# Optimization experiments

Measured on AMD Instinct MI355X. Metric: run time of the kernel, lower is better.

The kernel has to match this reference:

```python
import jax, jax.numpy as jnp
import numpy as np

NUM_HEADS = 12
SIZE_PER_HEAD = 64


def setup_inputs() -> dict:
    key = jax.random.key(0)
    ks = jax.random.split(key, 4)
    B, S, D = 4, 2048, NUM_HEADS * SIZE_PER_HEAD
    std = 0.02
    return {
        "x": jax.random.normal(ks[0], (B, S, D), dtype=jnp.float32),
        "Wq": jax.random.normal(ks[1], (D, D), dtype=jnp.float32) * std,
        "bq": jnp.zeros((D,), dtype=jnp.float32),
        "Wk": jax.random.normal(ks[2], (D, D), dtype=jnp.float32) * std,
        "bk": jnp.zeros((D,), dtype=jnp.float32),
        "Wv": jax.random.normal(ks[3], (D, D), dtype=jnp.float32) * std,
        "bv": jnp.zeros((D,), dtype=jnp.float32),
        "mask": jnp.ones((B, S), dtype=jnp.int32),
    }


def reference(x, Wq, bq, Wk, bk, Wv, bv, mask):
    B, S, Dm = x.shape
    H, Dh = NUM_HEADS, SIZE_PER_HEAD
    # QKV projections (no activation, per defaults)
    q = (x @ Wq + bq).reshape(B, S, H, Dh)
    k = (x @ Wk + bk).reshape(B, S, H, Dh)
    v = (x @ Wv + bv).reshape(B, S, H, Dh)
    # scaled dot-product scores [B, H, F, T]
    scores = jnp.einsum("bfhd,bthd->bhft", q, k) / jnp.sqrt(
        jnp.asarray(Dh, dtype=x.dtype)
    )
    # additive mask: (1 - mask) * -10000, broadcast over heads and F
    adder = (1.0 - mask.astype(x.dtype))[:, None, None, :] * -10000.0
    probs = jax.nn.softmax(scores + adder, axis=-1)
    # dropout is identity at inference (training=None)
    ctx = jnp.einsum("bhft,bthd->bfhd", probs, v)
    return ctx.reshape(B, S, H * Dh)
```

## Files before the change

kernel.cpp:

```cpp
#include <hip/hip_runtime.h>
#include <cstdint>
#include <cstddef>

#define B_  4
#define S_  2048
#define H_  12
#define DH  64
#define DM  768

typedef unsigned short u16;
typedef __bf16 bf16x8 __attribute__((ext_vector_type(8)));
typedef float f32x4 __attribute__((ext_vector_type(4)));

__device__ __forceinline__ u16 f2bf(float f) {
  unsigned u = __float_as_uint(f);
  u += 0x7FFFu + ((u >> 16) & 1u);
  return (u16)(u >> 16);
}

__device__ __forceinline__ void gl16(const u16* g, u16* l) {
  __builtin_amdgcn_global_load_lds((const __attribute__((address_space(1))) void*)g,
                                   (__attribute__((address_space(3))) void*)l,
                                   16, 0, 0);
}

__global__ __launch_bounds__(256) void k_prep(const float* __restrict__ x, u16* __restrict__ xb,
                                              const int* __restrict__ mask, int* __restrict__ mflags,
                                              const float* __restrict__ Wq, const float* __restrict__ Wk,
                                              const float* __restrict__ Wv, u16* __restrict__ Wt) {
  const int bid = blockIdx.x;
  if (bid < 6144) {
    int i = bid * 256 + threadIdx.x;
    const float4 v = ((const float4*)x)[i];
    ushort4 o;
    o.x = f2bf(v.x); o.y = f2bf(v.y); o.z = f2bf(v.z); o.w = f2bf(v.w);
    ((ushort4*)xb)[i] = o;
    if (bid < 64) {
      __shared__ int f;
      if (threadIdx.x == 0) f = 0;
      __syncthreads();
      if (threadIdx.x < 128 && mask[bid * 128 + threadIdx.x] != 1) f = 1;
      __syncthreads();
      if (threadIdx.x == 0) mflags[bid] = f;
    }
  } else {
    const int b2 = bid - 6144;
    const int z = b2 / 576, rem = b2 % 576;
    const int by = rem / 24, bx = rem % 24;
    const float* W = z == 0 ? Wq : (z == 1 ? Wk : Wv);
    u16* o = Wt + (size_t)z * DM * DM;
    __shared__ float t[32][33];
    const int xx = threadIdx.x & 31, yy = threadIdx.x >> 5;
    const int n0 = bx * 32, k0 = by * 32;
#pragma unroll
    for (int i = 0; i < 4; i++)
      t[yy + i*8][xx] = W[(size_t)(k0 + yy + i*8)*DM + n0 + xx];
    __syncthreads();
#pragma unroll
    for (int i = 0; i < 4; i++)
      o[(size_t)(n0 + yy + i*8)*DM + k0 + xx] = f2bf(t[xx][yy + i*8]);
  }
}

__global__ __launch_bounds__(256, 2) void k_qkv(const u16* __restrict__ Xb, const u16* __restrict__ Wt,
                                                const float* __restrict__ bq, const float* __restrict__ bk,
                                                const float* __restrict__ bv, u16* __restrict__ QKV,
                                                u16* __restrict__ Vt) {
  const int n0 = blockIdx.x * 256, m0 = blockIdx.y * 128;
  const int mat = blockIdx.x / 3;
  const int n0r = n0 - mat * 768;
  const float* bias = mat == 0 ? bq : (mat == 1 ? bk : bv);
  __shared__ __align__(16) u16 Al[2*128*32];
  __shared__ __align__(16) u16 Bl[2*256*32];
  const int tid = threadIdx.x, w = tid >> 6, l = tid & 63, l15 = l & 15, quad = l >> 4;
  const int wm = w & 1, wn = w >> 1;
  f32x4 acc[4][8];
#pragma unroll
  for (int i = 0; i < 4; i++)
#pragma unroll
    for (int j = 0; j < 8; j++) acc[i][j] = f32x4{0.f, 0.f, 0.f, 0.f};

  int aoff[2], boff[4];
#pragma unroll
  for (int i = 0; i < 2; i++) {
    int c = tid + i*256;
    int r = c >> 2, s = c & 3, sl = s ^ ((r ^ (r >> 2)) & 3);
    aoff[i] = r*DM + sl*8;
  }
#pragma unroll
  for (int i = 0; i < 4; i++) {
    int c = tid + i*256;
    int r = c >> 2, s = c & 3, sl = s ^ ((r ^ (r >> 2)) & 3);
    boff[i] = r*DM + sl*8;
  }
  const u16* ap = Xb + (size_t)m0 * DM;
  const u16* bp = Wt + (size_t)n0 * DM;

#define STAGE(kt) {                                             \
    int ab = ((kt) & 1) * 4096, bb = ((kt) & 1) * 8192;         \
    _Pragma("unroll")                                           \
    for (int i = 0; i < 2; i++)                                 \
      gl16(ap + (kt)*32 + aoff[i], Al + ab + (tid + i*256)*8);  \
    _Pragma("unroll")                                           \
    for (int i = 0; i < 4; i++)                                 \
      gl16(bp + (kt)*32 + boff[i], Bl + bb + (tid + i*256)*8);  \
  }

  STAGE(0)
  for (int kt = 0; kt < DM/32; ++kt) {
    __syncthreads();
    if (kt + 1 < DM/32) STAGE(kt+1)
    const int ab = (kt & 1) * 4096, bb = (kt & 1) * 8192;
    bf16x8 af[4], bfr[8];
#pragma unroll
    for (int mt = 0; mt < 4; mt++) {
      int row = wm*64 + mt*16 + l15;
      int ph = quad ^ ((row ^ (row >> 2)) & 3);
      af[mt] = *(const bf16x8*)(Al + ab + row*32 + ph*8);
    }
#pragma unroll
    for (int nt = 0; nt < 8; nt++) {
      int row = wn*128 + nt*16 + l15;
      int ph = quad ^ ((row ^ (row >> 2)) & 3);
      bfr[nt] = *(const bf16x8*)(Bl + bb + row*32 + ph*8);
    }
#pragma unroll
    for (int mt = 0; mt < 4; mt++)
#pragma unroll
      for (int nt = 0; nt < 8; nt++)
        acc[mt][nt] = __builtin_amdgcn_mfma_f32_16x16x32_bf16(af[mt], bfr[nt], acc[mt][nt], 0, 0, 0);
  }
#undef STAGE

  float b8[8];
#pragma unroll
  for (int nt = 0; nt < 8; nt++) b8[nt] = bias[n0r + wn*128 + nt*16 + l15];

  if (mat == 2) {
#pragma unroll
    for (int mt = 0; mt < 4; mt++) {
      int gm = m0 + wm*64 + mt*16 + quad*4;
      int b = gm >> 11, t = gm & 2047;
#pragma unroll
      for (int nt = 0; nt < 8; nt++) {
        int ng = n0r + wn*128 + nt*16;
        int h = ng >> 6, d = (ng & 63) + l15;
        ushort4 o;
        o.x = f2bf(acc[mt][nt][0] + b8[nt]);
        o.y = f2bf(acc[mt][nt][1] + b8[nt]);
        o.z = f2bf(acc[mt][nt][2] + b8[nt]);
        o.w = f2bf(acc[mt][nt][3] + b8[nt]);
        *(ushort4*)(Vt + ((size_t)(b*H_ + h)*DH + d)*S_ + t) = o;
      }
    }
  } else {
    const float osc = (mat == 0) ? (0.125f * 1.44269504f) : 1.0f;
    u16* outm = QKV + (size_t)mat * (size_t)(B_*S_) * DM;
#pragma unroll
    for (int mt = 0; mt < 4; mt++)
#pragma unroll
      for (int r = 0; r < 4; r++) {
        int gm = m0 + wm*64 + mt*16 + quad*4 + r;
        u16* orow = outm + (size_t)gm*DM + n0r + wn*128;
#pragma unroll
        for (int nt = 0; nt < 8; nt++)
          orow[nt*16 + l15] = f2bf((acc[mt][nt][r] + b8[nt]) * osc);
      }
  }
}

__global__ __launch_bounds__(256, 2) void k_attn(const u16* __restrict__ Qb, const u16* __restrict__ Kb,
                                                 const u16* __restrict__ Vt, const int* __restrict__ mask,
                                                 const int* __restrict__ mflags, float* __restrict__ out) {
  const int bh = blockIdx.x, b = bh / H_, h = bh % H_;
  const int q0 = blockIdx.y * 256;
  __shared__ __align__(16) u16 Kl[128*64];
  __shared__ __align__(16) u16 Vl[64*128];
  __shared__ __align__(16) u16 QP[4*64*72];
  __shared__ __align__(16) float maskl[128];
  const int tid = threadIdx.x, w = tid >> 6, l = tid & 63, l15 = l & 15, quad = l >> 4;

#pragma unroll
  for (int i = 0; i < 8; i++) {
    int c = tid + i*256;
    int r = c >> 3, s = c & 7, sl = s ^ (r & 7);
    gl16(Qb + (size_t)(b*S_ + q0 + r)*DM + h*DH + sl*8, QP + c*8);
  }
  __syncthreads();
  bf16x8 qf[4][2];
#pragma unroll
  for (int nt = 0; nt < 4; nt++)
#pragma unroll
    for (int ks = 0; ks < 2; ks++) {
      int r = w*64 + nt*16 + l15;
      int ph = (ks*4 + quad) ^ (r & 7);
      qf[nt][ks] = *(const bf16x8*)(QP + r*64 + ph*8);
    }
  __syncthreads();

  f32x4 O[4][4], Ol[4];
#pragma unroll
  for (int i = 0; i < 4; i++) {
    Ol[i] = f32x4{0.f, 0.f, 0.f, 0.f};
#pragma unroll
    for (int j = 0; j < 4; j++) O[i][j] = f32x4{0.f, 0.f, 0.f, 0.f};
  }
  const f32x4 ZV = {0.f, 0.f, 0.f, 0.f};
  bf16x8 vone;
#pragma unroll
  for (int j = 0; j < 8; j++) vone[j] = (l15 == 0) ? (__bf16)1.0f : (__bf16)0.0f;
  u16* Pw = QP + w*64*72;

  int koff[4], voff[4];
#pragma unroll
  for (int i = 0; i < 4; i++) {
    int c = tid + i*256;
    { int r = c >> 3, s = c & 7, sl = s ^ (r & 7);   koff[i] = r*DM + sl*8; }
    { int r = c >> 4, s = c & 15, sl = s ^ (r & 15); voff[i] = r*S_ + sl*8; }
  }
  const u16* kp = Kb + (size_t)(b*S_)*DM + h*DH;
  const u16* vp = Vt + (size_t)bh*DH*S_;

  for (int tt = 0; tt < S_/128; ++tt) {
    __syncthreads();
#pragma unroll
    for (int i = 0; i < 4; i++) {
      int c = tid + i*256;
      gl16(kp + koff[i], Kl + c*8);
      gl16(vp + voff[i], Vl + c*8);
    }
    kp += 128*DM; vp += 128;
    const int mflag = mflags[b*16 + tt];
    if (mflag && tid < 128)
      maskl[tid] = (1.0f - (float)mask[b*S_ + tt*128 + tid]) * (-10000.0f * 1.44269504f);
    __syncthreads();

#pragma unroll
    for (int h2 = 0; h2 < 2; ++h2) {
      f32x4 sc[4][4];
#pragma unroll
      for (int mt = 0; mt < 4; mt++) {
        int row = h2*64 + mt*16 + l15;
        bf16x8 k0f = *(const bf16x8*)(Kl + row*64 + ((quad    ) ^ (row & 7))*8);
        bf16x8 k1f = *(const bf16x8*)(Kl + row*64 + ((4 + quad) ^ (row & 7))*8);
#pragma unroll
        for (int nt = 0; nt < 4; nt++) {
          sc[mt][nt] = __builtin_amdgcn_mfma_f32_16x16x32_bf16(k0f, qf[nt][0], ZV, 0, 0, 0);
          sc[mt][nt] = __builtin_amdgcn_mfma_f32_16x16x32_bf16(k1f, qf[nt][1], sc[mt][nt], 0, 0, 0);
        }
      }
      if (mflag) {
#pragma unroll
        for (int mt = 0; mt < 4; mt++) {
          f32x4 mv = *(const f32x4*)&maskl[h2*64 + mt*16 + quad*4];
#pragma unroll
          for (int nt = 0; nt < 4; nt++)
#pragma unroll
            for (int r = 0; r < 4; r++) sc[mt][nt][r] += mv[r];
        }
      }
#pragma unroll
      for (int nt = 0; nt < 4; nt++)
#pragma unroll
        for (int mt = 0; mt < 4; mt++) {
          unsigned u[4];
#pragma unroll
          for (int r = 0; r < 4; r++) u[r] = __float_as_uint(__builtin_amdgcn_exp2f(sc[mt][nt][r]));
          uint2 pk;
          pk.x = __builtin_amdgcn_perm(u[1], u[0], 0x07060302u);
          pk.y = __builtin_amdgcn_perm(u[3], u[2], 0x07060302u);
          *(uint2*)(Pw + (nt*16 + l15)*72 + mt*16 + quad*4) = pk;
        }
      asm volatile("s_waitcnt lgkmcnt(0)" ::: "memory");
#pragma unroll
      for (int kk = 0; kk < 2; kk++) {
        int ksg = h2*2 + kk;
        bf16x8 pa[4], vb[4];
#pragma unroll
        for (int mo = 0; mo < 4; mo++)
          pa[mo] = *(const bf16x8*)(Pw + (mo*16 + l15)*72 + kk*32 + quad*8);
#pragma unroll
        for (int nd = 0; nd < 4; nd++) {
          int d = nd*16 + l15;
          int ph = (ksg*4 + quad) ^ (d & 15);
          vb[nd] = *(const bf16x8*)(Vl + d*128 + ph*8);
        }
#pragma unroll
        for (int mo = 0; mo < 4; mo++) {
#pragma unroll
          for (int nd = 0; nd < 4; nd++)
            O[mo][nd] = __builtin_amdgcn_mfma_f32_16x16x32_bf16(pa[mo], vb[nd], O[mo][nd], 0, 0, 0);
          Ol[mo] = __builtin_amdgcn_mfma_f32_16x16x32_bf16(pa[mo], vone, Ol[mo], 0, 0, 0);
        }
      }
    }
  }

#pragma unroll
  for (int mo = 0; mo < 4; mo++)
#pragma unroll
    for (int r = 0; r < 4; r++) {
      float lsum = __shfl(Ol[mo][r], l & 48);
      float inv = 1.0f / lsum;
      int q = q0 + w*64 + mo*16 + quad*4 + r;
      float* orow = out + (size_t)(b*S_ + q)*DM + h*DH;
#pragma unroll
      for (int nd = 0; nd < 4; nd++)
        orow[nd*16 + l15] = O[mo][nd][r] * inv;
    }
}

extern "C" void kernel_launch(void* const* d_in, const int* in_sizes, int n_in,
                              void* d_out, int out_size, void* d_ws, size_t ws_size,
                              hipStream_t stream) {
  const float* x  = (const float*)d_in[0];
  const float* Wq = (const float*)d_in[1];
  const float* bq = (const float*)d_in[2];
  const float* Wk = (const float*)d_in[3];
  const float* bk = (const float*)d_in[4];
  const float* Wv = (const float*)d_in[5];
  const float* bv = (const float*)d_in[6];
  const int* mask = (const int*)d_in[7];
  float* out = (float*)d_out;

  u16* Xb  = (u16*)d_ws;
  u16* Wt  = Xb  + (size_t)B_*S_*DM;
  u16* QKV = Wt  + (size_t)3*DM*DM;
  u16* Vt  = QKV + (size_t)3*B_*S_*DM;
  int* mflags = (int*)(Vt + (size_t)B_*S_*DM);

  k_prep<<<dim3(6144 + 1728), dim3(256), 0, stream>>>(x, Xb, mask, mflags, Wq, Wk, Wv, Wt);
  k_qkv <<<dim3(9, 64), dim3(256), 0, stream>>>(Xb, Wt, bq, bk, bv, QKV, Vt);
  k_attn<<<dim3(B_*H_, S_/256), dim3(256), 0, stream>>>(QKV, QKV + (size_t)B_*S_*DM, Vt, mask, mflags, out);
}
```

Baseline: 222.1 us.

## Register-prefetch K/V and GEMM tiles, shrink QKV tiles with swizzled grid

The QKV GEMM moves from 128x256 double-buffered LDS tiles via global_load_lds to 128x128 single-buffered tiles. The next k-slice is prefetched into registers and written to LDS between two custom barriers. The grid is flattened to 1152 blocks with a grouped tile order for L2 reuse, and occupancy is raised to 4 blocks per CU. The attention kernel likewise switches K/V loading to register prefetch of the next tile, issued before the Q load, and drops one barrier. This trades async LDS DMA for VGPR staging and extra LDS stores to overlap global latency with MFMA work.

```diff
diff --git a/kernel.cpp b/kernel.cpp
--- a/kernel.cpp
+++ b/kernel.cpp
@@ -23,6 +23,8 @@
                                    (__attribute__((address_space(3))) void*)l,
                                    16, 0, 0);
 }
+
+#define BAR() asm volatile("s_waitcnt lgkmcnt(0)\n\ts_barrier" ::: "memory")
 
 __global__ __launch_bounds__(256) void k_prep(const float* __restrict__ x, u16* __restrict__ xb,
                                               const int* __restrict__ mask, int* __restrict__ mflags,
@@ -62,97 +64,102 @@
   }
 }
 
-__global__ __launch_bounds__(256, 2) void k_qkv(const u16* __restrict__ Xb, const u16* __restrict__ Wt,
+__global__ __launch_bounds__(256, 4) void k_qkv(const u16* __restrict__ Xb, const u16* __restrict__ Wt,
                                                 const float* __restrict__ bq, const float* __restrict__ bk,
                                                 const float* __restrict__ bv, u16* __restrict__ QKV,
                                                 u16* __restrict__ Vt) {
-  const int n0 = blockIdx.x * 256, m0 = blockIdx.y * 128;
-  const int mat = blockIdx.x / 3;
-  const int n0r = n0 - mat * 768;
+  const int f = blockIdx.x;
+  const int mat = f / 384;
+  const int g = f % 384;
+  const int j = g >> 3;
+  const int m0 = ((g & 7) * 8 + (j / 6)) * 128;
+  const int n0 = (j % 6) * 128;
   const float* bias = mat == 0 ? bq : (mat == 1 ? bk : bv);
-  __shared__ __align__(16) u16 Al[2*128*32];
-  __shared__ __align__(16) u16 Bl[2*256*32];
+  __shared__ __align__(16) u16 Al[128*32];
+  __shared__ __align__(16) u16 Bl[128*32];
   const int tid = threadIdx.x, w = tid >> 6, l = tid & 63, l15 = l & 15, quad = l >> 4;
   const int wm = w & 1, wn = w >> 1;
-  f32x4 acc[4][8];
+  f32x4 acc[4][4];
 #pragma unroll
   for (int i = 0; i < 4; i++)
 #pragma unroll
-    for (int j = 0; j < 8; j++) acc[i][j] = f32x4{0.f, 0.f, 0.f, 0.f};
-
-  int aoff[2], boff[4];
+    for (int jj = 0; jj < 4; jj++) acc[i][jj] = f32x4{0.f, 0.f, 0.f, 0.f};
+
+  int aoff[2];
 #pragma unroll
   for (int i = 0; i < 2; i++) {
     int c = tid + i*256;
     int r = c >> 2, s = c & 3, sl = s ^ ((r ^ (r >> 2)) & 3);
     aoff[i] = r*DM + sl*8;
   }
-#pragma unroll
-  for (int i = 0; i < 4; i++) {
-    int c = tid + i*256;
-    int r = c >> 2, s = c & 3, sl = s ^ ((r ^ (r >> 2)) & 3);
-    boff[i] = r*DM + sl*8;
-  }
   const u16* ap = Xb + (size_t)m0 * DM;
-  const u16* bp = Wt + (size_t)n0 * DM;
-
-#define STAGE(kt) {                                             \
-    int ab = ((kt) & 1) * 4096, bb = ((kt) & 1) * 8192;         \
-    _Pragma("unroll")                                           \
-    for (int i = 0; i < 2; i++)                                 \
-      gl16(ap + (kt)*32 + aoff[i], Al + ab + (tid + i*256)*8);  \
-    _Pragma("unroll")                                           \
-    for (int i = 0; i < 4; i++)                                 \
-      gl16(bp + (kt)*32 + boff[i], Bl + bb + (tid + i*256)*8);  \
-  }
-
-  STAGE(0)
+  const u16* bp = Wt + ((size_t)mat * DM + n0) * DM;
+
+  int4 ra[2], rb[2];
+#pragma unroll
+  for (int i = 0; i < 2; i++) {
+    ra[i] = *(const int4*)(ap + aoff[i]);
+    rb[i] = *(const int4*)(bp + aoff[i]);
+  }
+  ap += 32; bp += 32;
+
   for (int kt = 0; kt < DM/32; ++kt) {
-    __syncthreads();
-    if (kt + 1 < DM/32) STAGE(kt+1)
-    const int ab = (kt & 1) * 4096, bb = (kt & 1) * 8192;
-    bf16x8 af[4], bfr[8];
+    BAR();
+#pragma unroll
+    for (int i = 0; i < 2; i++) {
+      *(int4*)(Al + (tid + i*256)*8) = ra[i];
+      *(int4*)(Bl + (tid + i*256)*8) = rb[i];
+    }
+    if (kt + 1 < DM/32) {
+#pragma unroll
+      for (int i = 0; i < 2; i++) {
+        ra[i] = *(const int4*)(ap + aoff[i]);
+        rb[i] = *(const int4*)(bp + aoff[i]);
+      }
+      ap += 32; bp += 32;
+    }
+    BAR();
+    bf16x8 af[4], bfr[4];
 #pragma unroll
     for (int mt = 0; mt < 4; mt++) {
       int row = wm*64 + mt*16 + l15;
       int ph = quad ^ ((row ^ (row >> 2)) & 3);
-      af[mt] = *(const bf16x8*)(Al + ab + row*32 + ph*8);
-    }
-#pragma unroll
-    for (int nt = 0; nt < 8; nt++) {
-      int row = wn*128 + nt*16 + l15;
+      af[mt] = *(const bf16x8*)(Al + row*32 + ph*8);
+    }
+#pragma unroll
+    for (int nt = 0; nt < 4; nt++) {
+      int row = wn*64 + nt*16 + l15;
       int ph = quad ^ ((row ^ (row >> 2)) & 3);
-      bfr[nt] = *(const bf16x8*)(Bl + bb + row*32 + ph*8);
+      bfr[nt] = *(const bf16x8*)(Bl + row*32 + ph*8);
     }
 #pragma unroll
     for (int mt = 0; mt < 4; mt++)
 #pragma unroll
-      for (int nt = 0; nt < 8; nt++)
+      for (int nt = 0; nt < 4; nt++)
         acc[mt][nt] = __builtin_amdgcn_mfma_f32_16x16x32_bf16(af[mt], bfr[nt], acc[mt][nt], 0, 0, 0);
   }
-#undef STAGE
-
-  float b8[8];
-#pragma unroll
-  for (int nt = 0; nt < 8; nt++) b8[nt] = bias[n0r + wn*128 + nt*16 + l15];
+
+  float b4[4];
+#pragma unroll
+  for (int nt = 0; nt < 4; nt++) b4[nt] = bias[n0 + wn*64 + nt*16 + l15];
 
   if (mat == 2) {
-#pragma unroll
-    for (int mt = 0; mt < 4; mt++) {
-      int gm = m0 + wm*64 + mt*16 + quad*4;
-      int b = gm >> 11, t = gm & 2047;
-#pragma unroll
-      for (int nt = 0; nt < 8; nt++) {
-        int ng = n0r + wn*128 + nt*16;
-        int h = ng >> 6, d = (ng & 63) + l15;
+    const int b = m0 >> 11;
+    const int h = (n0 + wn*64) >> 6;
+    const int tbase = (m0 & 2047) + wm*64;
+#pragma unroll
+    for (int mt = 0; mt < 4; mt++)
+#pragma unroll
+      for (int nt = 0; nt < 4; nt++) {
+        int d = nt*16 + l15;
+        int t = tbase + mt*16 + quad*4;
         ushort4 o;
-        o.x = f2bf(acc[mt][nt][0] + b8[nt]);
-        o.y = f2bf(acc[mt][nt][1] + b8[nt]);
-        o.z = f2bf(acc[mt][nt][2] + b8[nt]);
-        o.w = f2bf(acc[mt][nt][3] + b8[nt]);
+        o.x = f2bf(acc[mt][nt][0] + b4[nt]);
+        o.y = f2bf(acc[mt][nt][1] + b4[nt]);
+        o.z = f2bf(acc[mt][nt][2] + b4[nt]);
+        o.w = f2bf(acc[mt][nt][3] + b4[nt]);
         *(ushort4*)(Vt + ((size_t)(b*H_ + h)*DH + d)*S_ + t) = o;
       }
-    }
   } else {
     const float osc = (mat == 0) ? (0.125f * 1.44269504f) : 1.0f;
     u16* outm = QKV + (size_t)mat * (size_t)(B_*S_) * DM;
@@ -161,10 +168,10 @@
 #pragma unroll
       for (int r = 0; r < 4; r++) {
         int gm = m0 + wm*64 + mt*16 + quad*4 + r;
-        u16* orow = outm + (size_t)gm*DM + n0r + wn*128;
-#pragma unroll
-        for (int nt = 0; nt < 8; nt++)
-          orow[nt*16 + l15] = f2bf((acc[mt][nt][r] + b8[nt]) * osc);
+        u16* orow = outm + (size_t)gm*DM + n0 + wn*64;
+#pragma unroll
+        for (int nt = 0; nt < 4; nt++)
+          orow[nt*16 + l15] = f2bf((acc[mt][nt][r] + b4[nt]) * osc);
       }
   }
 }
@@ -180,6 +187,24 @@
   __shared__ __align__(16) float maskl[128];
   const int tid = threadIdx.x, w = tid >> 6, l = tid & 63, l15 = l & 15, quad = l >> 4;
 
+  int koff[4], voff[4];
+#pragma unroll
+  for (int i = 0; i < 4; i++) {
+    int c = tid + i*256;
+    { int r = c >> 3, s = c & 7, sl = s ^ (r & 7);   koff[i] = r*DM + sl*8; }
+    { int r = c >> 4, s = c & 15, sl = s ^ (r & 15); voff[i] = r*S_ + sl*8; }
+  }
+  const u16* kp = Kb + (size_t)(b*S_)*DM + h*DH;
+  const u16* vp = Vt + (size_t)bh*DH*S_;
+
+  int4 rk[4], rv[4];
+#pragma unroll
+  for (int i = 0; i < 4; i++) {
+    rk[i] = *(const int4*)(kp + koff[i]);
+    rv[i] = *(const int4*)(vp + voff[i]);
+  }
+  kp += 128*DM; vp += 128;
+
 #pragma unroll
   for (int i = 0; i < 8; i++) {
     int c = tid + i*256;
@@ -196,44 +221,39 @@
       int ph = (ks*4 + quad) ^ (r & 7);
       qf[nt][ks] = *(const bf16x8*)(QP + r*64 + ph*8);
     }
-  __syncthreads();
 
   f32x4 O[4][4], Ol[4];
 #pragma unroll
   for (int i = 0; i < 4; i++) {
     Ol[i] = f32x4{0.f, 0.f, 0.f, 0.f};
 #pragma unroll
-    for (int j = 0; j < 4; j++) O[i][j] = f32x4{0.f, 0.f, 0.f, 0.f};
+    for (int jj = 0; jj < 4; jj++) O[i][jj] = f32x4{0.f, 0.f, 0.f, 0.f};
   }
   const f32x4 ZV = {0.f, 0.f, 0.f, 0.f};
   bf16x8 vone;
 #pragma unroll
-  for (int j = 0; j < 8; j++) vone[j] = (l15 == 0) ? (__bf16)1.0f : (__bf16)0.0f;
+  for (int jj = 0; jj < 8; jj++) vone[jj] = (l15 == 0) ? (__bf16)1.0f : (__bf16)0.0f;
   u16* Pw = QP + w*64*72;
 
-  int koff[4], voff[4];
-#pragma unroll
-  for (int i = 0; i < 4; i++) {
-    int c = tid + i*256;
-    { int r = c >> 3, s = c & 7, sl = s ^ (r & 7);   koff[i] = r*DM + sl*8; }
-    { int r = c >> 4, s = c & 15, sl = s ^ (r & 15); voff[i] = r*S_ + sl*8; }
-  }
-  const u16* kp = Kb + (size_t)(b*S_)*DM + h*DH;
-  const u16* vp = Vt + (size_t)bh*DH*S_;
-
   for (int tt = 0; tt < S_/128; ++tt) {
-    __syncthreads();
+    BAR();
 #pragma unroll
     for (int i = 0; i < 4; i++) {
-      int c = tid + i*256;
-      gl16(kp + koff[i], Kl + c*8);
-      gl16(vp + voff[i], Vl + c*8);
-    }
-    kp += 128*DM; vp += 128;
+      *(int4*)(Kl + (tid + i*256)*8) = rk[i];
+      *(int4*)(Vl + (tid + i*256)*8) = rv[i];
+    }
+    if (tt + 1 < S_/128) {
+#pragma unroll
+      for (int i = 0; i < 4; i++) {
+        rk[i] = *(const int4*)(kp + koff[i]);
+        rv[i] = *(const int4*)(vp + voff[i]);
+      }
+      kp += 128*DM; vp += 128;
+    }
     const int mflag = mflags[b*16 + tt];
     if (mflag && tid < 128)
       maskl[tid] = (1.0f - (float)mask[b*S_ + tt*128 + tid]) * (-10000.0f * 1.44269504f);
-    __syncthreads();
+    BAR();
 
 #pragma unroll
     for (int h2 = 0; h2 < 2; ++h2) {
@@ -330,6 +350,6 @@
   int* mflags = (int*)(Vt + (size_t)B_*S_*DM);
 
   k_prep<<<dim3(6144 + 1728), dim3(256), 0, stream>>>(x, Xb, mask, mflags, Wq, Wk, Wv, Wt);
-  k_qkv <<<dim3(9, 64), dim3(256), 0, stream>>>(Xb, Wt, bq, bk, bv, QKV, Vt);
+  k_qkv <<<dim3(1152), dim3(256), 0, stream>>>(Xb, Wt, bq, bk, bv, QKV, Vt);
   k_attn<<<dim3(B_*H_, S_/256), dim3(256), 0, stream>>>(QKV, QKV + (size_t)B_*S_*DM, Vt, mask, mflags, out);
 }
```

Result: slower. 324.8 us (+46.3%).

## Read K/V fragments directly from global memory and shrink attention blocks

Applied to the files above, without the earlier changes.

The attention kernel no longer stages K and V tiles in shared memory. Each wave now loads its MFMA fragments straight from global memory, and the mask is read directly instead of through an LDS buffer. Blocks shrink to 128 threads (two waves, 128 queries) with twice as many blocks, which removes the per-tile barriers and most of the LDS footprint. The trade-off is that each wave issues redundant global/L2 loads for the same K/V data with no cross-wave reuse, and the V reads along S with a stride of S_ may be poorly coalesced.

```diff
diff --git a/kernel.cpp b/kernel.cpp
--- a/kernel.cpp
+++ b/kernel.cpp
@@ -161,28 +161,26 @@
 #pragma unroll
       for (int r = 0; r < 4; r++) {
         int gm = m0 + wm*64 + mt*16 + quad*4 + r;
-        u16* orow = outm + (size_t)gm*DM + n0r + wn*128;
+        u16* orow = QKV + (size_t)mat * (size_t)(B_*S_) * DM + (size_t)gm*DM + n0r + wn*128;
 #pragma unroll
         for (int nt = 0; nt < 8; nt++)
           orow[nt*16 + l15] = f2bf((acc[mt][nt][r] + b8[nt]) * osc);
       }
-  }
-}
-
-__global__ __launch_bounds__(256, 2) void k_attn(const u16* __restrict__ Qb, const u16* __restrict__ Kb,
-                                                 const u16* __restrict__ Vt, const int* __restrict__ mask,
-                                                 const int* __restrict__ mflags, float* __restrict__ out) {
+    (void)outm;
+  }
+}
+
+__global__ __launch_bounds__(128) void k_attn(const u16* __restrict__ Qb, const u16* __restrict__ Kb,
+                                              const u16* __restrict__ Vt, const int* __restrict__ mask,
+                                              const int* __restrict__ mflags, float* __restrict__ out) {
   const int bh = blockIdx.x, b = bh / H_, h = bh % H_;
-  const int q0 = blockIdx.y * 256;
-  __shared__ __align__(16) u16 Kl[128*64];
-  __shared__ __align__(16) u16 Vl[64*128];
-  __shared__ __align__(16) u16 QP[4*64*72];
-  __shared__ __align__(16) float maskl[128];
+  const int q0 = blockIdx.y * 128;
+  __shared__ __align__(16) u16 QP[2*64*72];
   const int tid = threadIdx.x, w = tid >> 6, l = tid & 63, l15 = l & 15, quad = l >> 4;
 
 #pragma unroll
   for (int i = 0; i < 8; i++) {
-    int c = tid + i*256;
+    int c = tid + i*128;
     int r = c >> 3, s = c & 7, sl = s ^ (r & 7);
     gl16(Qb + (size_t)(b*S_ + q0 + r)*DM + h*DH + sl*8, QP + c*8);
   }
@@ -211,38 +209,23 @@
   for (int j = 0; j < 8; j++) vone[j] = (l15 == 0) ? (__bf16)1.0f : (__bf16)0.0f;
   u16* Pw = QP + w*64*72;
 
-  int koff[4], voff[4];
-#pragma unroll
-  for (int i = 0; i < 4; i++) {
-    int c = tid + i*256;
-    { int r = c >> 3, s = c & 7, sl = s ^ (r & 7);   koff[i] = r*DM + sl*8; }
-    { int r = c >> 4, s = c & 15, sl = s ^ (r & 15); voff[i] = r*S_ + sl*8; }
-  }
   const u16* kp = Kb + (size_t)(b*S_)*DM + h*DH;
   const u16* vp = Vt + (size_t)bh*DH*S_;
+  const int* mrow = mask + b*S_;
+  const float MASKC = -10000.0f * 1.44269504f;
 
   for (int tt = 0; tt < S_/128; ++tt) {
-    __syncthreads();
-#pragma unroll
-    for (int i = 0; i < 4; i++) {
-      int c = tid + i*256;
-      gl16(kp + koff[i], Kl + c*8);
-      gl16(vp + voff[i], Vl + c*8);
-    }
-    kp += 128*DM; vp += 128;
+    const int t0 = tt * 128;
     const int mflag = mflags[b*16 + tt];
-    if (mflag && tid < 128)
-      maskl[tid] = (1.0f - (float)mask[b*S_ + tt*128 + tid]) * (-10000.0f * 1.44269504f);
-    __syncthreads();
 
 #pragma unroll
     for (int h2 = 0; h2 < 2; ++h2) {
       f32x4 sc[4][4];
 #pragma unroll
       for (int mt = 0; mt < 4; mt++) {
-        int row = h2*64 + mt*16 + l15;
-        bf16x8 k0f = *(const bf16x8*)(Kl + row*64 + ((quad    ) ^ (row & 7))*8);
-        bf16x8 k1f = *(const bf16x8*)(Kl + row*64 + ((4 + quad) ^ (row & 7))*8);
+        const u16* krow = kp + (size_t)(t0 + h2*64 + mt*16 + l15)*DM;
+        bf16x8 k0f = *(const bf16x8*)(krow + quad*8);
+        bf16x8 k1f = *(const bf16x8*)(krow + 32 + quad*8);
 #pragma unroll
         for (int nt = 0; nt < 4; nt++) {
           sc[mt][nt] = __builtin_amdgcn_mfma_f32_16x16x32_bf16(k0f, qf[nt][0], ZV, 0, 0, 0);
@@ -252,7 +235,12 @@
       if (mflag) {
 #pragma unroll
         for (int mt = 0; mt < 4; mt++) {
-          f32x4 mv = *(const f32x4*)&maskl[h2*64 + mt*16 + quad*4];
+          int4 m4 = *(const int4*)(mrow + t0 + h2*64 + mt*16 + quad*4);
+          f32x4 mv;
+          mv[0] = (1.0f - (float)m4.x) * MASKC;
+          mv[1] = (1.0f - (float)m4.y) * MASKC;
+          mv[2] = (1.0f - (float)m4.z) * MASKC;
+          mv[3] = (1.0f - (float)m4.w) * MASKC;
 #pragma unroll
           for (int nt = 0; nt < 4; nt++)
 #pragma unroll
@@ -280,11 +268,8 @@
         for (int mo = 0; mo < 4; mo++)
           pa[mo] = *(const bf16x8*)(Pw + (mo*16 + l15)*72 + kk*32 + quad*8);
 #pragma unroll
-        for (int nd = 0; nd < 4; nd++) {
-          int d = nd*16 + l15;
-          int ph = (ksg*4 + quad) ^ (d & 15);
-          vb[nd] = *(const bf16x8*)(Vl + d*128 + ph*8);
-        }
+        for (int nd = 0; nd < 4; nd++)
+          vb[nd] = *(const bf16x8*)(vp + (size_t)(nd*16 + l15)*S_ + t0 + ksg*32 + quad*8);
 #pragma unroll
         for (int mo = 0; mo < 4; mo++) {
 #pragma unroll
@@ -331,5 +316,5 @@
 
   k_prep<<<dim3(6144 + 1728), dim3(256), 0, stream>>>(x, Xb, mask, mflags, Wq, Wk, Wv, Wt);
   k_qkv <<<dim3(9, 64), dim3(256), 0, stream>>>(Xb, Wt, bq, bk, bv, QKV, Vt);
-  k_attn<<<dim3(B_*H_, S_/256), dim3(256), 0, stream>>>(QKV, QKV + (size_t)B_*S_*DM, Vt, mask, mflags, out);
-}
+  k_attn<<<dim3(B_*H_, S_/128), dim3(128), 0, stream>>>(QKV, QKV + (size_t)B_*S_*DM, Vt, mask, mflags, out);
+}
```

After: 314.2 us. 41.5% more time.
